# Kernel tuning notes

Measured on AMD Instinct MI355X. Metric: run time of the kernel, lower is better.

The kernel has to match this reference:

```python
import jax, jax.numpy as jnp
import numpy as np

B, S, D = 4, 4096, 1024  # batch, seq_len, input_dim == state_dim


def setup_inputs() -> dict:
    key = jax.random.key(0)
    ks = jax.random.split(key, 5)
    x = jax.random.normal(ks[0], (B, S, D), dtype=jnp.float32)
    h0 = jnp.zeros((B, D), dtype=jnp.float32)
    dt_w = jax.random.normal(ks[1], (D, D), dtype=jnp.float32) * 0.02
    dt_b = jnp.ones((D,), dtype=jnp.float32)  # torch init: bias.fill_(1.0)
    A_log = jax.random.normal(ks[2], (D,), dtype=jnp.float32) * 0.5 - 1.0
    B_w = jax.random.normal(ks[3], (D, D), dtype=jnp.float32) * 0.02
    C_w = jax.random.normal(ks[4], (D, D), dtype=jnp.float32) * 0.02
    Dp = jnp.zeros((D,), dtype=jnp.float32)
    return {"x": x, "h0": h0, "dt_w": dt_w, "dt_b": dt_b, "A_log": A_log,
            "B_w": B_w, "C_w": C_w, "D": Dp}


def reference(x, h0, dt_w, dt_b, A_log, B_w, C_w, D):
    # dt = softplus(x @ dt_w^T + dt_b): [B,S,D]
    dt = jax.nn.softplus(jnp.einsum('bsd,ed->bse', x, dt_w) + dt_b)
    A = -jnp.exp(A_log)                       # [D], negative -> gate in (0,1)
    Bp = jnp.einsum('bsd,ed->bse', x, B_w)    # [B,S,D]
    gate = jnp.exp(dt * A)                    # [B,S,D]
    inputs = dt * Bp * x                      # [B,S,D] (requires state_dim==input_dim)
    # fold initial state into first step: h_1 = gate_1*h0 + in_1
    inputs = inputs.at[:, 0].add(gate[:, 0] * h0)
    # associative scan for h_t = gate_t * h_{t-1} + in_t
    def comb(c1, c2):
        a1, b1 = c1
        a2, b2 = c2
        return (a1 * a2, a2 * b1 + b2)
    _, h_all = jax.lax.associative_scan(comb, (gate, inputs), axis=1)
    out = jnp.einsum('bse,de->bsd', h_all, C_w) + D * x
    return out
```

## Files before the change

### kernel.cpp

```cpp
#include <hip/hip_runtime.h>
#include <hip/hip_bf16.h>
#include <stdint.h>
#include <stddef.h>


#define Bdim 4
#define Sdim 4096
#define Dd   1024
#define Mdim (Bdim * Sdim)
#define CCH  128
#define LCH  (Sdim / CCH)

typedef __attribute__((ext_vector_type(8))) short  short8;
typedef __attribute__((ext_vector_type(4))) short  short4v;
typedef __attribute__((ext_vector_type(4))) float  floatx4;

__device__ __forceinline__ float b2f(short v) {
  unsigned u = ((unsigned)(unsigned short)v) << 16;
  float f; __builtin_memcpy(&f, &u, 4); return f;
}
__device__ __forceinline__ short f2b(float f) {
  unsigned u; __builtin_memcpy(&u, &f, 4);
  u += 0x7fffu + ((u >> 16) & 1u);
  return (short)(u >> 16);
}

__device__ __forceinline__ short8 ld8f(const float* p) {
  floatx4 lo = *(const floatx4*)p;
  floatx4 hi = *(const floatx4*)(p + 4);
  short8 r;
  r[0] = f2b(lo[0]); r[1] = f2b(lo[1]); r[2] = f2b(lo[2]); r[3] = f2b(lo[3]);
  r[4] = f2b(hi[0]); r[5] = f2b(hi[1]); r[6] = f2b(hi[2]); r[7] = f2b(hi[3]);
  return r;
}

__device__ __forceinline__ void st_out(short* p, float v) { *p = f2b(v); }
__device__ __forceinline__ void st_out(float* p, float v) { *p = v; }

__device__ __forceinline__ void cp16(const void* g, void* l) {
  __builtin_amdgcn_global_load_lds(
      (__attribute__((address_space(1))) void*)g,
      (__attribute__((address_space(3))) void*)l, 16, 0, 0);
}


#define STGA(bufB, h, kk) do { \
  cp16(Ag + (size_t)((h) * 64) * lda + (kk), \
       smc + (bufB) + ((h) * 64 + ldsArow) * 128); \
  cp16(Ag + (size_t)((h) * 64 + 128) * lda + (kk), \
       smc + (bufB) + ((h) * 64 + 128 + ldsArow) * 128); \
} while (0)

#define STGB(bufB, h, kk) do { \
  cp16(Bg + (size_t)((h) * 32) * ldw + (kk), \
       smc + (bufB) + ((h) * 32 + ldsBrow) * 128); \
  cp16(Bg + (size_t)((h) * 32 + 128) * ldw + (kk), \
       smc + (bufB) + ((h) * 32 + 128 + ldsBrow) * 128); \
} while (0)

#define LDA4(bufB, mh) do { \
  _Pragma("unroll") \
  for (int mf = 0; mf < 4; ++mf) { \
    const char* p_ = smc + (bufB) + (wm + (mh) * 64 + mf * 16 + l16) * 128; \
    a[mf][0] = *(const short8*)(p_ + c0x); \
    a[mf][1] = *(const short8*)(p_ + c1x); \
  } \
} while (0)

#define LDB2(bufB, nh, bb) do { \
  _Pragma("unroll") \
  for (int g = 0; g < 2; ++g) { \
    const char* p_ = smc + (bufB) + (wn + (nh) * 32 + g * 16 + l16) * 128; \
    bb[g][0] = *(const short8*)(p_ + c0x); \
    bb[g][1] = *(const short8*)(p_ + c1x); \
  } \
} while (0)

#define MM8(mh, nh, bb) do { \
  __builtin_amdgcn_s_setprio(1); \
  _Pragma("unroll") \
  for (int mf = 0; mf < 4; ++mf) { \
    _Pragma("unroll") \
    for (int g = 0; g < 2; ++g) { \
      floatx4 c_ = acc[(mh) * 4 + mf][(nh) * 2 + g]; \
      c_ = __builtin_amdgcn_mfma_f32_16x16x32_bf16(a[mf][0], bb[g][0], c_, 0, 0, 0); \
      c_ = __builtin_amdgcn_mfma_f32_16x16x32_bf16(a[mf][1], bb[g][1], c_, 0, 0, 0); \
      acc[(mh) * 4 + mf][(nh) * 2 + g] = c_; \
    } \
  } \
  __builtin_amdgcn_s_setprio(0); \
  __builtin_amdgcn_sched_barrier(0); \
} while (0)

#define WBAR(n) asm volatile("s_waitcnt vmcnt(" n ")\n\ts_barrier" ::: "memory")
#define BARO()  asm volatile("s_barrier" ::: "memory")

template <typename OT, bool FUSE>
__global__ __launch_bounds__(512, 2) void gemm8(
    const short* __restrict__ A, int lda,
    const short* __restrict__ W, int ldw,
    OT* __restrict__ Out, int ldo, int K,
    const float* __restrict__ Dp, const short* __restrict__ Xr, int ldx)
{
  __shared__ short smem[65536];
  char* smc = (char*)smem;

  const int tid  = threadIdx.x;
  const int lane = tid & 63, wv = tid >> 6;
  const int quad = lane >> 4, l16 = lane & 15;
  const int wm = (wv & 1) << 7;
  const int wn = (wv >> 1) << 6;
  const int m0 = blockIdx.x << 8;
  const int n0 = blockIdx.y << 8;

  const int sx  = (l16 & 7) << 4;
  const int c0x = (quad << 4) ^ sx;
  const int c1x = (64 + (quad << 4)) ^ sx;

  const int r0 = tid >> 3;
  const int sk = (((tid & 7) ^ (r0 & 7)) << 3);
  const short* Ag = A + (size_t)(m0 + r0) * lda + sk;
  const short* Bg = W + (size_t)(n0 + ((r0 >> 5) << 6) + (r0 & 31)) * ldw + sk;
  const int ldsArow = wv << 3;
  const int ldsBrow = ((wv >> 2) << 6) + ((wv << 3) & 31);

  short8 a[4][2], b0[2][2], b1[2][2];
  floatx4 acc[8][4] = {};

  STGA(0, 0, 0);
  STGB(65536, 0, 0);
  STGB(65536, 1, 0);
  STGA(0, 1, 0);

  const int NT = K >> 6;
  for (int t = 0; t < NT; ++t) {
    const int cb   = t & 1;
    const int ab   = cb << 15;
    const int bbuf = 65536 + ab;
    const int an   = (cb ^ 1) << 15;
    const int bn   = 65536 + an;
    const int kk   = (t + 1) << 6;
    const bool st  = (t + 1) < NT;

    WBAR("4");
    LDA4(ab, 0);
    LDB2(bbuf, 0, b0);
    if (st) STGA(an, 0, kk);
    MM8(0, 0, b0);

    if (st) WBAR("4"); else WBAR("2");
    LDB2(bbuf, 1, b1);
    if (st) STGB(bn, 0, kk);
    MM8(0, 1, b1);

    if (st) WBAR("4"); else WBAR("0");
    LDA4(ab, 1);
    if (st) STGB(bn, 1, kk);
    MM8(1, 1, b1);

    BARO();
    if (st) STGA(an, 1, kk);
    MM8(1, 0, b0);
  }

#pragma unroll
  for (int i = 0; i < 8; ++i) {
#pragma unroll
    for (int j = 0; j < 4; ++j) {
#pragma unroll
      for (int r = 0; r < 4; ++r) {
        int m = m0 + wm + i * 16 + quad * 4 + r;
        int n = n0 + wn + j * 16 + l16;
        float v = acc[i][j][r];
        if (FUSE) v += Dp[n] * b2f(Xr[(size_t)m * ldx + n]);
        st_out(Out + (size_t)m * ldo + n, v);
      }
    }
  }
}

__global__ __launch_bounds__(256) void cast_all(
    const float* __restrict__ x, const float* __restrict__ dt_w,
    const float* __restrict__ B_w, const float* __restrict__ C_w,
    short* __restrict__ xb, short* __restrict__ wcat)
{
  size_t i = ((size_t)blockIdx.x * 256 + threadIdx.x) * 8;
  const size_t NX = (size_t)Mdim * Dd;
  const size_t NW = (size_t)Dd * Dd;
  if (i < NX) {
    *(short8*)(xb + i) = ld8f(x + i);
  } else {
    size_t j = i - NX;
    const float* src = (j < NW) ? (dt_w + j)
                     : (j < 2 * NW) ? (B_w + (j - NW))
                                    : (C_w + (j - 2 * NW));
    *(short8*)(wcat + j) = ld8f(src);
  }
}

__device__ __forceinline__ void gate_in(float dtp, float db, float nA,
                                        float bp, float xv,
                                        float& g, float& u) {
  float z  = dtp + db;
  float sp = fmaxf(z, 0.f) + log1pf(expf(-fabsf(z)));
  g = expf(sp * nA);
  u = sp * bp * xv;
}

__global__ __launch_bounds__(256) void scan_local(
    short* __restrict__ P, const short* __restrict__ xb,
    const float* __restrict__ dt_b, const float* __restrict__ A_log,
    const float* __restrict__ h0,
    float* __restrict__ Pc, float* __restrict__ Hl)
{
  const int b  = blockIdx.x >> 7;
  const int c  = blockIdx.x & 127;
  const int d0 = threadIdx.x * 4;

  floatx4 db = *(const floatx4*)(dt_b + d0);
  floatx4 al = *(const floatx4*)(A_log + d0);
  float nA[4], p[4] = {1.f, 1.f, 1.f, 1.f}, h[4] = {};
#pragma unroll
  for (int j = 0; j < 4; j++) nA[j] = -expf(al[j]);

  const size_t mrow = (size_t)b * Sdim + (size_t)c * LCH;
  for (int t = 0; t < LCH; t++) {
    size_t m = mrow + t;
    short4v dt4 = *(const short4v*)(P + m * 2048 + d0);
    short4v bp4 = *(const short4v*)(P + m * 2048 + 1024 + d0);
    short4v xv4 = *(const short4v*)(xb + m * Dd + d0);
    short4v hl4, pg4;
#pragma unroll
    for (int j = 0; j < 4; j++) {
      float g, u;
      gate_in(b2f(dt4[j]), db[j], nA[j], b2f(bp4[j]), b2f(xv4[j]), g, u);
      if (c == 0 && t == 0) u += g * h0[b * Dd + d0 + j];
      h[j] = g * h[j] + u;
      p[j] *= g;
      hl4[j] = f2b(h[j]);
      pg4[j] = f2b(p[j]);
    }
    *(short4v*)(P + m * 2048 + d0)        = hl4;
    *(short4v*)(P + m * 2048 + 1024 + d0) = pg4;
  }
  size_t o = ((size_t)b * CCH + c) * Dd + d0;
  *(floatx4*)(Pc + o) = floatx4{p[0], p[1], p[2], p[3]};
  *(floatx4*)(Hl + o) = floatx4{h[0], h[1], h[2], h[3]};
}

__global__ __launch_bounds__(256) void scan_carry4(
    float* __restrict__ Pc, const float* __restrict__ Hl)
{
  const int t  = blockIdx.x * 256 + threadIdx.x;
  const int b  = t >> 8;
  const int d0 = (t & 255) * 4;
  floatx4 st = {};
  for (int c = 0; c < CCH; c++) {
    size_t o = ((size_t)b * CCH + c) * Dd + d0;
    floatx4 pv = *(const floatx4*)(Pc + o);
    floatx4 hv = *(const floatx4*)(Hl + o);
    *(floatx4*)(Pc + o) = st;
    st = pv * st + hv;
  }
}

__global__ __launch_bounds__(256) void scan_fix(
    short* __restrict__ P, const float* __restrict__ carry)
{
  size_t idx = ((size_t)blockIdx.x * 256 + threadIdx.x) * 4;
  const int m  = (int)(idx >> 10);
  const int d0 = (int)(idx & 1023);
  const int b  = m >> 12;
  const int c  = (m & (Sdim - 1)) >> 5;
  short4v hl4 = *(const short4v*)(P + (size_t)m * 2048 + d0);
  short4v pg4 = *(const short4v*)(P + (size_t)m * 2048 + 1024 + d0);
  floatx4 cv  = *(const floatx4*)(carry + ((size_t)b * CCH + c) * Dd + d0);
  short4v o4;
#pragma unroll
  for (int j = 0; j < 4; j++)
    o4[j] = f2b(b2f(hl4[j]) + cv[j] * b2f(pg4[j]));
  *(short4v*)(P + (size_t)m * 2048 + d0) = o4;
}

extern "C" void kernel_launch(void* const* d_in, const int* in_sizes, int n_in,
                              void* d_out, int out_size, void* d_ws, size_t ws_size,
                              hipStream_t stream)
{
  const float* x     = (const float*)d_in[0];
  const float* h0    = (const float*)d_in[1];
  const float* dt_w  = (const float*)d_in[2];
  const float* dt_b  = (const float*)d_in[3];
  const float* A_log = (const float*)d_in[4];
  const float* B_w   = (const float*)d_in[5];
  const float* C_w   = (const float*)d_in[6];
  const float* Dp    = (const float*)d_in[7];
  float* out = (float*)d_out;

  char* ws = (char*)d_ws;
  short* P    = (short*)(ws);
  short* xb   = (short*)(ws + (64ull  << 20));
  short* wcat = (short*)(ws + (96ull  << 20));
  float* Pc   = (float*)(ws + (102ull << 20));
  float* Hl   = (float*)(ws + (104ull << 20));

  cast_all<<<9728, 256, 0, stream>>>(x, dt_w, B_w, C_w, xb, wcat);

  gemm8<short, false><<<dim3(Mdim / 256, 2048 / 256), 512, 0, stream>>>(
      xb, Dd, wcat, Dd, P, 2048, 1024, nullptr, nullptr, 0);

  scan_local<<<Bdim * CCH, 256, 0, stream>>>(P, xb, dt_b, A_log, h0, Pc, Hl);
  scan_carry4<<<4, 256, 0, stream>>>(Pc, Hl);
  scan_fix<<<(Mdim * Dd / 4) / 256, 256, 0, stream>>>(P, Pc);

  gemm8<float, true><<<dim3(Mdim / 256, 1024 / 256), 512, 0, stream>>>(
      P, 2048, wcat + 2 * 1024 * 1024, Dd, out, Dd, 1024, Dp, xb, Dd);
}
```

Baseline: 354.0 us.

## Widen scan parallelism, use fast exp2/log2 softplus, prefetch, and widen carry kernel

The local scan now gives each thread one channel instead of four, and the grid gains a second dimension, so four times as many wavefronts are available to hide latency. The next step's inputs are prefetched one iteration ahead. Softplus and the gate are computed with hardware exp2/log2 intrinsics, which drops log1p and the abs/max branch, and the carry kernel is spread across 64 blocks with loads batched in groups of eight. The costs are scalar 2-byte memory accesses instead of 8-byte vectors, some loss of precision in softplus, and possible overflow of exp2 for large z.

```diff
diff --git a/kernel.cpp b/kernel.cpp
--- a/kernel.cpp
+++ b/kernel.cpp
@@ -15,14 +15,26 @@
 typedef __attribute__((ext_vector_type(4))) short  short4v;
 typedef __attribute__((ext_vector_type(4))) float  floatx4;
 
+#if __has_builtin(__builtin_amdgcn_exp2f)
+#define EXP2(x) __builtin_amdgcn_exp2f(x)
+#else
+#define EXP2(x) exp2f(x)
+#endif
+#if __has_builtin(__builtin_amdgcn_logf)
+#define LOG2(x) __builtin_amdgcn_logf(x)
+#else
+#define LOG2(x) __log2f(x)
+#endif
+#define LOG2E 1.44269504088896f
+#define LN2   0.69314718055995f
+
 __device__ __forceinline__ float b2f(short v) {
   unsigned u = ((unsigned)(unsigned short)v) << 16;
   float f; __builtin_memcpy(&f, &u, 4); return f;
 }
 __device__ __forceinline__ short f2b(float f) {
-  unsigned u; __builtin_memcpy(&u, &f, 4);
-  u += 0x7fffu + ((u >> 16) & 1u);
-  return (short)(u >> 16);
+  __hip_bfloat16 h = __float2bfloat16(f);
+  short s; __builtin_memcpy(&s, &h, 2); return s;
 }
 
 __device__ __forceinline__ short8 ld8f(const float* p) {
@@ -42,7 +54,6 @@
       (__attribute__((address_space(1))) void*)g,
       (__attribute__((address_space(3))) void*)l, 16, 0, 0);
 }
-
 
 #define STGA(bufB, h, kk) do { \
   cp16(Ag + (size_t)((h) * 64) * lda + (kk), \
@@ -198,69 +209,70 @@
   }
 }
 
-__device__ __forceinline__ void gate_in(float dtp, float db, float nA,
-                                        float bp, float xv,
-                                        float& g, float& u) {
-  float z  = dtp + db;
-  float sp = fmaxf(z, 0.f) + log1pf(expf(-fabsf(z)));
-  g = expf(sp * nA);
-  u = sp * bp * xv;
-}
-
 __global__ __launch_bounds__(256) void scan_local(
     short* __restrict__ P, const short* __restrict__ xb,
     const float* __restrict__ dt_b, const float* __restrict__ A_log,
     const float* __restrict__ h0,
     float* __restrict__ Pc, float* __restrict__ Hl)
 {
-  const int b  = blockIdx.x >> 7;
-  const int c  = blockIdx.x & 127;
-  const int d0 = threadIdx.x * 4;
-
-  floatx4 db = *(const floatx4*)(dt_b + d0);
-  floatx4 al = *(const floatx4*)(A_log + d0);
-  float nA[4], p[4] = {1.f, 1.f, 1.f, 1.f}, h[4] = {};
-#pragma unroll
-  for (int j = 0; j < 4; j++) nA[j] = -expf(al[j]);
+  const int b = blockIdx.x >> 7;
+  const int c = blockIdx.x & 127;
+  const int d = blockIdx.y * 256 + threadIdx.x;
+
+  const float db = dt_b[d];
+  const float nA = -EXP2(A_log[d] * LOG2E);
 
   const size_t mrow = (size_t)b * Sdim + (size_t)c * LCH;
-  for (int t = 0; t < LCH; t++) {
-    size_t m = mrow + t;
-    short4v dt4 = *(const short4v*)(P + m * 2048 + d0);
-    short4v bp4 = *(const short4v*)(P + m * 2048 + 1024 + d0);
-    short4v xv4 = *(const short4v*)(xb + m * Dd + d0);
-    short4v hl4, pg4;
-#pragma unroll
-    for (int j = 0; j < 4; j++) {
-      float g, u;
-      gate_in(b2f(dt4[j]), db[j], nA[j], b2f(bp4[j]), b2f(xv4[j]), g, u);
-      if (c == 0 && t == 0) u += g * h0[b * Dd + d0 + j];
-      h[j] = g * h[j] + u;
-      p[j] *= g;
-      hl4[j] = f2b(h[j]);
-      pg4[j] = f2b(p[j]);
+  short* pp = P + mrow * 2048 + d;
+  const short* px = xb + mrow * 1024 + d;
+
+  float p = 1.f, h = 0.f;
+  short dt_c = pp[0], bp_c = pp[1024], xv_c = px[0];
+  for (int t = 0; t < LCH; ++t) {
+    short dt_n = 0, bp_n = 0, xv_n = 0;
+    if (t + 1 < LCH) {
+      dt_n = pp[2048]; bp_n = pp[2048 + 1024]; xv_n = px[1024];
     }
-    *(short4v*)(P + m * 2048 + d0)        = hl4;
-    *(short4v*)(P + m * 2048 + 1024 + d0) = pg4;
-  }
-  size_t o = ((size_t)b * CCH + c) * Dd + d0;
-  *(floatx4*)(Pc + o) = floatx4{p[0], p[1], p[2], p[3]};
-  *(floatx4*)(Hl + o) = floatx4{h[0], h[1], h[2], h[3]};
-}
-
-__global__ __launch_bounds__(256) void scan_carry4(
+    float z  = b2f(dt_c) + db;
+    float e  = EXP2(z * LOG2E);
+    float L  = LOG2(1.f + e);
+    float sp = LN2 * L;
+    float g  = EXP2(nA * L);
+    float u  = sp * b2f(bp_c) * b2f(xv_c);
+    if (c == 0 && t == 0) u += g * h0[b * Dd + d];
+    h = g * h + u;
+    p *= g;
+    pp[0]    = f2b(h);
+    pp[1024] = f2b(p);
+    pp += 2048; px += 1024;
+    dt_c = dt_n; bp_c = bp_n; xv_c = xv_n;
+  }
+  size_t o = ((size_t)b * CCH + c) * Dd + d;
+  Pc[o] = p;
+  Hl[o] = h;
+}
+
+__global__ __launch_bounds__(64) void scan_carry(
     float* __restrict__ Pc, const float* __restrict__ Hl)
 {
-  const int t  = blockIdx.x * 256 + threadIdx.x;
-  const int b  = t >> 8;
-  const int d0 = (t & 255) * 4;
-  floatx4 st = {};
-  for (int c = 0; c < CCH; c++) {
-    size_t o = ((size_t)b * CCH + c) * Dd + d0;
-    floatx4 pv = *(const floatx4*)(Pc + o);
-    floatx4 hv = *(const floatx4*)(Hl + o);
-    *(floatx4*)(Pc + o) = st;
-    st = pv * st + hv;
+  const int t = blockIdx.x * 64 + threadIdx.x;
+  const int b = t >> 10;
+  const int d = t & 1023;
+  const size_t base = (size_t)b * CCH * Dd + d;
+  float st = 0.f;
+  for (int cg = 0; cg < CCH; cg += 8) {
+    float pv[8], hv[8];
+#pragma unroll
+    for (int j = 0; j < 8; ++j) {
+      size_t o = base + (size_t)(cg + j) * Dd;
+      pv[j] = Pc[o]; hv[j] = Hl[o];
+    }
+#pragma unroll
+    for (int j = 0; j < 8; ++j) {
+      size_t o = base + (size_t)(cg + j) * Dd;
+      Pc[o] = st;
+      st = pv[j] * st + hv[j];
+    }
   }
 }
 
@@ -308,8 +320,9 @@
   gemm8<short, false><<<dim3(Mdim / 256, 2048 / 256), 512, 0, stream>>>(
       xb, Dd, wcat, Dd, P, 2048, 1024, nullptr, nullptr, 0);
 
-  scan_local<<<Bdim * CCH, 256, 0, stream>>>(P, xb, dt_b, A_log, h0, Pc, Hl);
-  scan_carry4<<<4, 256, 0, stream>>>(Pc, Hl);
+  scan_local<<<dim3(Bdim * CCH, Dd / 256), 256, 0, stream>>>(
+      P, xb, dt_b, A_log, h0, Pc, Hl);
+  scan_carry<<<64, 64, 0, stream>>>(Pc, Hl);
   scan_fix<<<(Mdim * Dd / 4) / 256, 256, 0, stream>>>(P, Pc);
 
   gemm8<float, true><<<dim3(Mdim / 256, 1024 / 256), 512, 0, stream>>>(
```

Result: faster. 287.9 us (-18.7%).
